# Kernel tuning notes

Hardware: AMD Instinct MI355X
Metric: run time of the kernel (lower is better)

## Reference

```python
import jax, jax.numpy as jnp
import numpy as np

NEG_SLOPE = 0.2  # PyG GATConv default


def gat_layer(x, W, att_src, att_dst, bias, src, dst, num_nodes, heads, out_ch):
    # x: [N, Fin]; W: [Fin, heads*out_ch]; att_*: [heads, out_ch]; bias: [heads*out_ch]
    xw = (x @ W).reshape(num_nodes, heads, out_ch)          # [N, H, C]
    a_src = jnp.sum(xw * att_src, axis=-1)                  # [N, H]
    a_dst = jnp.sum(xw * att_dst, axis=-1)                  # [N, H]
    e = jax.nn.leaky_relu(a_src[src] + a_dst[dst], NEG_SLOPE)  # [E, H]
    # segment softmax over incoming edges of each destination node
    e_max = jax.ops.segment_max(e, dst, num_segments=num_nodes)   # [N, H]
    e_exp = jnp.exp(e - e_max[dst])                                # [E, H]
    denom = jax.ops.segment_sum(e_exp, dst, num_segments=num_nodes)
    alpha = e_exp / denom[dst]                                     # [E, H]
    out = jax.ops.segment_sum(alpha[:, :, None] * xw[src], dst, num_segments=num_nodes)  # [N, H, C]
    return out.reshape(num_nodes, heads * out_ch) + bias


def setup_inputs() -> dict:
    key = jax.random.key(0)
    ks = jax.random.split(key, 12)
    N, E = 50000, 800000
    F_IN, HID, HEADS, NCLS = 128, 32, 4, 8
    x = jax.random.normal(ks[0], (N, F_IN), dtype=jnp.float32)
    src = jax.random.randint(ks[1], (E,), 0, N)
    dst = jax.random.randint(ks[2], (E,), 0, N)
    dst = jnp.where(dst == src, (dst + 1) % N, dst)  # no self loops; reference adds them
    edge_index = jnp.stack([src, dst]).astype(jnp.int64)
    s1 = 1.0 / np.sqrt(F_IN)
    s2 = 1.0 / np.sqrt(HEADS * HID)
    W1 = jax.random.normal(ks[3], (F_IN, HEADS * HID), dtype=jnp.float32) * s1
    att_src1 = jax.random.normal(ks[4], (HEADS, HID), dtype=jnp.float32) * s2
    att_dst1 = jax.random.normal(ks[5], (HEADS, HID), dtype=jnp.float32) * s2
    b1 = jnp.zeros((HEADS * HID,), dtype=jnp.float32)
    W2 = jax.random.normal(ks[6], (HEADS * HID, NCLS), dtype=jnp.float32) * s2
    att_src2 = jax.random.normal(ks[7], (1, NCLS), dtype=jnp.float32)
    att_dst2 = jax.random.normal(ks[8], (1, NCLS), dtype=jnp.float32)
    b2 = jnp.zeros((NCLS,), dtype=jnp.float32)
    return {"x": x, "edge_index": edge_index, "W1": W1, "att_src1": att_src1,
            "att_dst1": att_dst1, "b1": b1, "W2": W2, "att_src2": att_src2,
            "att_dst2": att_dst2, "b2": b2}


def reference(x, edge_index, W1, att_src1, att_dst1, b1, W2, att_src2, att_dst2, b2):
    N = x.shape[0]
    loops = jnp.arange(N, dtype=edge_index.dtype)
    src = jnp.concatenate([edge_index[0], loops])  # add self loops (PyG default)
    dst = jnp.concatenate([edge_index[1], loops])
    h = gat_layer(x, W1, att_src1, att_dst1, b1, src, dst, N, heads=4, out_ch=32)
    h = jax.nn.relu(h)
    out = gat_layer(h, W2, att_src2, att_dst2, b2, src, dst, N, heads=1, out_ch=8)
    return jax.nn.log_softmax(out, axis=1)
```

## Files before the change

kernel.cpp:

```cpp
#include <hip/hip_runtime.h>
#include <hip/hip_fp16.h>
#include <math.h>

#define F_IN   128
#define HEADS  4
#define HID    32
#define NCLS   8
#define SLOPE  0.2f
#define CAP    64
#define NBK    256
#define BSH    8
#define CHK    4096
#define BCAP   5120

typedef _Float16 half8 __attribute__((ext_vector_type(8)));
typedef float    floatx4 __attribute__((ext_vector_type(4)));
typedef float    floatv4 __attribute__((ext_vector_type(4)));

__global__ void k_prep(int* __restrict__ bcur,
                       const float* __restrict__ W1, _Float16* __restrict__ Wt) {
    if (blockIdx.x == 0) {
        bcur[threadIdx.x] = threadIdx.x * BCAP;
    } else {
        int idx = (blockIdx.x - 1) * 256 + threadIdx.x;
        int c = idx >> 7, k = idx & 127;
        Wt[c * 128 + k] = (_Float16)W1[k * 128 + c];
    }
}

__global__ void k_scatter(const int* __restrict__ ei, int* __restrict__ bcur,
                          unsigned* __restrict__ stage, int E) {
    __shared__ int hist[NBK];
    __shared__ int lcur[NBK];
    hist[threadIdx.x] = 0;
    int probe = ei[2 * (threadIdx.x & 63) + 1];
    bool is64 = (__ballot(probe != 0) == 0ULL);
    __syncthreads();
    int base = blockIdx.x * CHK;
    int dd[16], ss[16];
    #pragma unroll
    for (int k = 0; k < 16; k++) {
        int i = base + k * 256 + threadIdx.x;
        if (i < E) {
            dd[k] = is64 ? ei[2 * E + 2 * i] : ei[E + i];
            ss[k] = is64 ? ei[2 * i]         : ei[i];
            atomicAdd(&hist[dd[k] >> BSH], 1);
        } else dd[k] = -1;
    }
    __syncthreads();
    {
        int h = hist[threadIdx.x];
        lcur[threadIdx.x] = (h > 0) ? atomicAdd(&bcur[threadIdx.x], h) : 0;
    }
    __syncthreads();
    #pragma unroll
    for (int k = 0; k < 16; k++) {
        if (dd[k] >= 0) {
            int bkt = dd[k] >> BSH;
            int p = atomicAdd(&lcur[bkt], 1);
            if (p < (bkt + 1) * BCAP)
                stage[p] = ((unsigned)dd[k] << 16) | (unsigned)ss[k];
        }
    }
}

__global__ void k_bucket_gemm(const unsigned* __restrict__ stage,
                              const int* __restrict__ bcur,
                              unsigned short* __restrict__ csr16, int* __restrict__ cur,
                              int N,
                              const float* __restrict__ x, const _Float16* __restrict__ Wt,
                              const float* __restrict__ as1, const float* __restrict__ ad1,
                              _Float16* __restrict__ xwh, float* __restrict__ asrc,
                              float* __restrict__ adst) {
    if ((int)blockIdx.x < NBK) {
        int b  = blockIdx.x;
        int lo = b << BSH;
        if (lo >= N) return;
        int nn = N - lo; if (nn > 256) nn = 256;
        __shared__ int lc[256];
        lc[threadIdx.x] = (threadIdx.x < nn) ? 1 : 0;
        __syncthreads();
        if (threadIdx.x < nn)
            csr16[(size_t)(lo + threadIdx.x) * CAP] = (unsigned short)(lo + threadIdx.x);
        int base = b * BCAP;
        int cnt  = bcur[b] - base;
        if (cnt > BCAP) cnt = BCAP;
        if (cnt < 0) cnt = 0;
        for (int i = base + threadIdx.x; i < base + cnt; i += 256) {
            unsigned u = stage[i];
            int d = u >> 16, s = u & 0xFFFF;
            int p = atomicAdd(&lc[d - lo], 1);
            if (p < CAP) csr16[(size_t)d * CAP + p] = (unsigned short)s;
        }
        __syncthreads();
        if (threadIdx.x < nn) {
            int c = lc[threadIdx.x];
            cur[lo + threadIdx.x] = (c > CAP) ? CAP : c;
        }
        return;
    }
    int gb   = blockIdx.x - NBK;
    int wv   = threadIdx.x >> 6;
    int lane = threadIdx.x & 63;
    int r0   = gb * 64 + wv * 16;
    if (r0 >= N) return;
    int q = lane >> 4, t = lane & 15;
    int row = r0 + t;
    bool rok = row < N;

    half8 afr[4];
    #pragma unroll
    for (int kc = 0; kc < 4; kc++) {
        floatv4 u0 = {0.f, 0.f, 0.f, 0.f}, u1 = u0;
        if (rok) {
            const floatv4* xr = (const floatv4*)(x + (size_t)row * 128 + kc * 32 + q * 8);
            u0 = __builtin_nontemporal_load(xr);
            u1 = __builtin_nontemporal_load(xr + 1);
        }
        afr[kc][0] = (_Float16)u0[0]; afr[kc][1] = (_Float16)u0[1];
        afr[kc][2] = (_Float16)u0[2]; afr[kc][3] = (_Float16)u0[3];
        afr[kc][4] = (_Float16)u1[0]; afr[kc][5] = (_Float16)u1[1];
        afr[kc][6] = (_Float16)u1[2]; afr[kc][7] = (_Float16)u1[3];
    }

    float ps[4], pd[4];
    #pragma unroll
    for (int ct = 0; ct < 8; ct++) {
        floatx4 acc = {0.f, 0.f, 0.f, 0.f};
        #pragma unroll
        for (int kc = 0; kc < 4; kc++) {
            half8 bfr = *(const half8*)(Wt + (ct * 16 + t) * 128 + kc * 32 + q * 8);
            acc = __builtin_amdgcn_mfma_f32_16x16x32_f16(afr[kc], bfr, acc, 0, 0, 0);
        }
        int col = ct * 16 + t;
        float sa = as1[col], da = ad1[col];
        if ((ct & 1) == 0) {
            #pragma unroll
            for (int g = 0; g < 4; g++) { ps[g] = 0.f; pd[g] = 0.f; }
        }
        #pragma unroll
        for (int g = 0; g < 4; g++) {
            int r = r0 + q * 4 + g;
            if (r < N)
                __builtin_nontemporal_store((_Float16)acc[g], xwh + (size_t)r * 128 + col);
            ps[g] += acc[g] * sa;
            pd[g] += acc[g] * da;
        }
        if (ct & 1) {
            int h = ct >> 1;
            #pragma unroll
            for (int g = 0; g < 4; g++) {
                float a = ps[g], d = pd[g];
                a += __shfl_xor(a, 1); d += __shfl_xor(d, 1);
                a += __shfl_xor(a, 2); d += __shfl_xor(d, 2);
                a += __shfl_xor(a, 4); d += __shfl_xor(d, 4);
                a += __shfl_xor(a, 8); d += __shfl_xor(d, 8);
                int r = r0 + q * 4 + g;
                if (t == 0 && r < N) { asrc[r * 4 + h] = a; adst[r * 4 + h] = d; }
            }
        }
    }
}

__global__ void k_agg1(const _Float16* __restrict__ xwh, const float* __restrict__ asrc,
                       const float* __restrict__ adst, const int* __restrict__ cur,
                       const unsigned short* __restrict__ csr16, const float* __restrict__ b1,
                       const float* __restrict__ W2, const float* __restrict__ as2,
                       const float* __restrict__ ad2, float* __restrict__ xw2,
                       float* __restrict__ asrc2, float* __restrict__ adst2, int N) {
    int node = (blockIdx.x * blockDim.x + threadIdx.x) >> 6;
    int lane = threadIdx.x & 63;
    if (node >= N) return;
    int h = lane >> 4;
    int t = lane & 15;
    int ch = h * 32 + 2 * t;

    const float4* w2p = (const float4*)(W2 + ch * 8);
    float4 wa0 = w2p[0], wa1 = w2p[1];
    float4 wb0 = w2p[2], wb1 = w2p[3];
    float a_s = as2[lane & 7];
    float a_d = ad2[lane & 7];

    float adst_h = adst[node * 4 + h];
    int beg = node * CAP;
    int deg = cur[node];
    int end = beg + deg;

    float s = 0.f, a0 = 0.f, a1 = 0.f;
    int j = beg;
    for (; j + 8 <= end; j += 8) {
        ushort4 sA = *(const ushort4*)(csr16 + j);
        ushort4 sB = *(const ushort4*)(csr16 + j + 4);
        float e0 = asrc[sA.x * 4 + h] + adst_h;
        float e1 = asrc[sA.y * 4 + h] + adst_h;
        float e2 = asrc[sA.z * 4 + h] + adst_h;
        float e3 = asrc[sA.w * 4 + h] + adst_h;
        float e4 = asrc[sB.x * 4 + h] + adst_h;
        float e5 = asrc[sB.y * 4 + h] + adst_h;
        float e6 = asrc[sB.z * 4 + h] + adst_h;
        float e7 = asrc[sB.w * 4 + h] + adst_h;
        float2 f0 = __half22float2(*(const __half2*)(xwh + (size_t)sA.x * 128 + ch));
        float2 f1 = __half22float2(*(const __half2*)(xwh + (size_t)sA.y * 128 + ch));
        float2 f2 = __half22float2(*(const __half2*)(xwh + (size_t)sA.z * 128 + ch));
        float2 f3 = __half22float2(*(const __half2*)(xwh + (size_t)sA.w * 128 + ch));
        float2 f4 = __half22float2(*(const __half2*)(xwh + (size_t)sB.x * 128 + ch));
        float2 f5 = __half22float2(*(const __half2*)(xwh + (size_t)sB.y * 128 + ch));
        float2 f6 = __half22float2(*(const __half2*)(xwh + (size_t)sB.z * 128 + ch));
        float2 f7 = __half22float2(*(const __half2*)(xwh + (size_t)sB.w * 128 + ch));
        e0 = (e0 > 0.f) ? e0 : SLOPE * e0;   float p0 = __expf(e0);
        e1 = (e1 > 0.f) ? e1 : SLOPE * e1;   float p1 = __expf(e1);
        e2 = (e2 > 0.f) ? e2 : SLOPE * e2;   float p2 = __expf(e2);
        e3 = (e3 > 0.f) ? e3 : SLOPE * e3;   float p3 = __expf(e3);
        e4 = (e4 > 0.f) ? e4 : SLOPE * e4;   float p4 = __expf(e4);
        e5 = (e5 > 0.f) ? e5 : SLOPE * e5;   float p5 = __expf(e5);
        e6 = (e6 > 0.f) ? e6 : SLOPE * e6;   float p6 = __expf(e6);
        e7 = (e7 > 0.f) ? e7 : SLOPE * e7;   float p7 = __expf(e7);
        s  += (p0 + p1 + p2 + p3) + (p4 + p5 + p6 + p7);
        a0 += p0 * f0.x + p1 * f1.x + p2 * f2.x + p3 * f3.x
            + p4 * f4.x + p5 * f5.x + p6 * f6.x + p7 * f7.x;
        a1 += p0 * f0.y + p1 * f1.y + p2 * f2.y + p3 * f3.y
            + p4 * f4.y + p5 * f5.y + p6 * f6.y + p7 * f7.y;
    }
    for (; j < end; j++) {
        int s0 = csr16[j];
        float e0 = asrc[s0 * 4 + h] + adst_h;
        float2 f0 = __half22float2(*(const __half2*)(xwh + (size_t)s0 * 128 + ch));
        e0 = (e0 > 0.f) ? e0 : SLOPE * e0;
        float p0 = __expf(e0);
        s  += p0;
        a0 += p0 * f0.x;
        a1 += p0 * f0.y;
    }
    float inv = 1.f / s;
    float o0 = fmaxf(a0 * inv + b1[ch],     0.f);
    float o1 = fmaxf(a1 * inv + b1[ch + 1], 0.f);

    float p[8];
    p[0] = o0 * wa0.x + o1 * wb0.x;  p[1] = o0 * wa0.y + o1 * wb0.y;
    p[2] = o0 * wa0.z + o1 * wb0.z;  p[3] = o0 * wa0.w + o1 * wb0.w;
    p[4] = o0 * wa1.x + o1 * wb1.x;  p[5] = o0 * wa1.y + o1 * wb1.y;
    p[6] = o0 * wa1.z + o1 * wb1.z;  p[7] = o0 * wa1.w + o1 * wb1.w;
    float qq[4];
    #pragma unroll
    for (int b = 0; b < 4; b++) {
        float keepv = (lane & 1) ? p[2 * b + 1] : p[2 * b];
        float sendv = (lane & 1) ? p[2 * b]     : p[2 * b + 1];
        qq[b] = keepv + __shfl_xor(sendv, 1);
    }
    float r2[2];
    #pragma unroll
    for (int b = 0; b < 2; b++) {
        float keepv = (lane & 2) ? qq[2 * b + 1] : qq[2 * b];
        float sendv = (lane & 2) ? qq[2 * b]     : qq[2 * b + 1];
        r2[b] = keepv + __shfl_xor(sendv, 2);
    }
    {
        float keepv = (lane & 4) ? r2[1] : r2[0];
        float sendv = (lane & 4) ? r2[0] : r2[1];
        r2[0] = keepv + __shfl_xor(sendv, 4);
    }
    float f = r2[0];
    f += __shfl_xor(f, 8);
    f += __shfl_xor(f, 16);
    f += __shfl_xor(f, 32);
    if (lane < 8) xw2[node * 8 + lane] = f;
    float vs = f * a_s;
    float vd = f * a_d;
    vs += __shfl_xor(vs, 1); vs += __shfl_xor(vs, 2); vs += __shfl_xor(vs, 4);
    vd += __shfl_xor(vd, 1); vd += __shfl_xor(vd, 2); vd += __shfl_xor(vd, 4);
    if (lane == 0) { asrc2[node] = vs; adst2[node] = vd; }
}

__global__ void k_agg2(const float* __restrict__ xw2, const float* __restrict__ asrc2,
                       const float* __restrict__ adst2, const int* __restrict__ cur,
                       const unsigned short* __restrict__ csr16, const float* __restrict__ b2,
                       float* __restrict__ out, int N) {
    int node = (blockIdx.x * blockDim.x + threadIdx.x) >> 6;
    int lane = threadIdx.x & 63;
    if (node >= N) return;
    int slot = lane >> 3;
    int c    = lane & 7;
    float adst = adst2[node];
    int beg = node * CAP;
    int deg = cur[node];
    float s = 0.f, acc = 0.f;
    for (int j = slot; j < deg; j += 8) {
        int s0 = csr16[beg + j];
        float e0 = asrc2[s0] + adst;
        float v0 = xw2[s0 * 8 + c];
        e0 = (e0 > 0.f) ? e0 : SLOPE * e0;
        float p0 = __expf(e0);
        s   += p0;
        acc += p0 * v0;
    }
    #pragma unroll
    for (int mk = 8; mk < 64; mk <<= 1) {
        s   += __shfl_xor(s, mk);
        acc += __shfl_xor(acc, mk);
    }
    float o = acc / s + b2[c];
    float mxv = o;
    mxv = fmaxf(mxv, __shfl_xor(mxv, 1));
    mxv = fmaxf(mxv, __shfl_xor(mxv, 2));
    mxv = fmaxf(mxv, __shfl_xor(mxv, 4));
    float ex = __expf(o - mxv);
    float se = ex;
    se += __shfl_xor(se, 1); se += __shfl_xor(se, 2); se += __shfl_xor(se, 4);
    if (slot == 0) out[node * 8 + c] = o - mxv - __logf(se);
}

extern "C" void kernel_launch(void* const* d_in, const int* in_sizes, int n_in,
                              void* d_out, int out_size, void* d_ws, size_t ws_size,
                              hipStream_t stream) {
    const float* x   = (const float*)d_in[0];
    const int*   ei  = (const int*)d_in[1];
    const float* W1  = (const float*)d_in[2];
    const float* as1 = (const float*)d_in[3];
    const float* ad1 = (const float*)d_in[4];
    const float* b1  = (const float*)d_in[5];
    const float* W2  = (const float*)d_in[6];
    const float* as2 = (const float*)d_in[7];
    const float* ad2 = (const float*)d_in[8];
    const float* b2  = (const float*)d_in[9];
    float* out = (float*)d_out;

    int N = in_sizes[0] / F_IN;
    int E = in_sizes[1] / 2;
    int GB   = (N + 63) / 64;
    int NCHK = (E + CHK - 1) / CHK;

    char* p = (char*)d_ws;
    auto carve = [&](size_t bytes) { char* q = p; p += (bytes + 255) & ~(size_t)255; return (void*)q; };
    _Float16* xw1h = (_Float16*)carve((size_t)N * 128 * 2);
    _Float16* Wt   = (_Float16*)carve(128 * 128 * 2);
    float* asrc1 = (float*)carve((size_t)N * 4 * 4);
    float* adst1 = (float*)carve((size_t)N * 4 * 4);
    float* xw2   = (float*)carve((size_t)N * 8 * 4);
    float* asrc2 = (float*)carve((size_t)N * 4);
    float* adst2 = (float*)carve((size_t)N * 4);
    int*   cur   = (int*)carve((size_t)N * 4);
    int*   bcur  = (int*)carve(NBK * 4);
    unsigned* stage = (unsigned*)carve((size_t)NBK * BCAP * 4);
    unsigned short* csr16 = (unsigned short*)carve((size_t)N * CAP * 2);

    k_prep<<<65, 256, 0, stream>>>(bcur, W1, Wt);
    k_scatter<<<NCHK, 256, 0, stream>>>(ei, bcur, stage, E);
    k_bucket_gemm<<<NBK + GB, 256, 0, stream>>>(stage, bcur, csr16, cur, N,
                                                x, Wt, as1, ad1, xw1h, asrc1, adst1);
    k_agg1<<<(N + 3) / 4, 256, 0, stream>>>(xw1h, asrc1, adst1, cur, csr16, b1,
                                            W2, as2, ad2, xw2, asrc2, adst2, N);
    k_agg2<<<(N + 3) / 4, 256, 0, stream>>>(xw2, asrc2, adst2, cur, csr16, b2, out, N);
}
```

Measured before the change: 206.8 us.

## Co-schedule edge scatter with layer-1 GEMM and stage GEMM output via LDS

```diff
diff --git a/kernel.cpp b/kernel.cpp
--- a/kernel.cpp
+++ b/kernel.cpp
@@ -12,6 +12,7 @@
 #define BSH    8
 #define CHK    4096
 #define BCAP   5120
+#define SSTR   136
 
 typedef _Float16 half8 __attribute__((ext_vector_type(8)));
 typedef float    floatx4 __attribute__((ext_vector_type(4)));
@@ -28,78 +29,49 @@
     }
 }
 
-__global__ void k_scatter(const int* __restrict__ ei, int* __restrict__ bcur,
-                          unsigned* __restrict__ stage, int E) {
-    __shared__ int hist[NBK];
-    __shared__ int lcur[NBK];
-    hist[threadIdx.x] = 0;
-    int probe = ei[2 * (threadIdx.x & 63) + 1];
-    bool is64 = (__ballot(probe != 0) == 0ULL);
-    __syncthreads();
-    int base = blockIdx.x * CHK;
-    int dd[16], ss[16];
-    #pragma unroll
-    for (int k = 0; k < 16; k++) {
-        int i = base + k * 256 + threadIdx.x;
-        if (i < E) {
-            dd[k] = is64 ? ei[2 * E + 2 * i] : ei[E + i];
-            ss[k] = is64 ? ei[2 * i]         : ei[i];
-            atomicAdd(&hist[dd[k] >> BSH], 1);
-        } else dd[k] = -1;
-    }
-    __syncthreads();
-    {
-        int h = hist[threadIdx.x];
-        lcur[threadIdx.x] = (h > 0) ? atomicAdd(&bcur[threadIdx.x], h) : 0;
-    }
-    __syncthreads();
-    #pragma unroll
-    for (int k = 0; k < 16; k++) {
-        if (dd[k] >= 0) {
-            int bkt = dd[k] >> BSH;
-            int p = atomicAdd(&lcur[bkt], 1);
-            if (p < (bkt + 1) * BCAP)
-                stage[p] = ((unsigned)dd[k] << 16) | (unsigned)ss[k];
-        }
-    }
-}
-
-__global__ void k_bucket_gemm(const unsigned* __restrict__ stage,
-                              const int* __restrict__ bcur,
-                              unsigned short* __restrict__ csr16, int* __restrict__ cur,
-                              int N,
-                              const float* __restrict__ x, const _Float16* __restrict__ Wt,
-                              const float* __restrict__ as1, const float* __restrict__ ad1,
-                              _Float16* __restrict__ xwh, float* __restrict__ asrc,
-                              float* __restrict__ adst) {
-    if ((int)blockIdx.x < NBK) {
-        int b  = blockIdx.x;
-        int lo = b << BSH;
-        if (lo >= N) return;
-        int nn = N - lo; if (nn > 256) nn = 256;
-        __shared__ int lc[256];
-        lc[threadIdx.x] = (threadIdx.x < nn) ? 1 : 0;
+__global__ void k_scatter_gemm(const int* __restrict__ ei, int* __restrict__ bcur,
+                               unsigned* __restrict__ stage, int E, int N, int NCHK,
+                               const float* __restrict__ x, const _Float16* __restrict__ Wt,
+                               const float* __restrict__ as1, const float* __restrict__ ad1,
+                               _Float16* __restrict__ xwh, float* __restrict__ asrc,
+                               float* __restrict__ adst) {
+    __shared__ __align__(16) unsigned char smem[4 * 16 * SSTR * 2];
+    if ((int)blockIdx.x < NCHK) {
+        int* hist = (int*)smem;
+        int* lcur = hist + NBK;
+        hist[threadIdx.x] = 0;
+        int probe = ei[2 * (threadIdx.x & 63) + 1];
+        bool is64 = (__ballot(probe != 0) == 0ULL);
         __syncthreads();
-        if (threadIdx.x < nn)
-            csr16[(size_t)(lo + threadIdx.x) * CAP] = (unsigned short)(lo + threadIdx.x);
-        int base = b * BCAP;
-        int cnt  = bcur[b] - base;
-        if (cnt > BCAP) cnt = BCAP;
-        if (cnt < 0) cnt = 0;
-        for (int i = base + threadIdx.x; i < base + cnt; i += 256) {
-            unsigned u = stage[i];
-            int d = u >> 16, s = u & 0xFFFF;
-            int p = atomicAdd(&lc[d - lo], 1);
-            if (p < CAP) csr16[(size_t)d * CAP + p] = (unsigned short)s;
+        int base = blockIdx.x * CHK;
+        int dd[16], ss[16];
+        #pragma unroll
+        for (int k = 0; k < 16; k++) {
+            int i = base + k * 256 + threadIdx.x;
+            if (i < E) {
+                dd[k] = is64 ? ei[2 * E + 2 * i] : ei[E + i];
+                ss[k] = is64 ? ei[2 * i]         : ei[i];
+                atomicAdd(&hist[dd[k] >> BSH], 1);
+            } else dd[k] = -1;
         }
         __syncthreads();
-        if (threadIdx.x < nn) {
-            int c = lc[threadIdx.x];
-            cur[lo + threadIdx.x] = (c > CAP) ? CAP : c;
+        {
+            int h = hist[threadIdx.x];
+            lcur[threadIdx.x] = (h > 0) ? atomicAdd(&bcur[threadIdx.x], h) : 0;
+        }
+        __syncthreads();
+        #pragma unroll
+        for (int k = 0; k < 16; k++) {
+            if (dd[k] >= 0) {
+                int bkt = dd[k] >> BSH;
+                int p = atomicAdd(&lcur[bkt], 1);
+                if (p < (bkt + 1) * BCAP)
+                    stage[p] = ((unsigned)dd[k] << 16) | (unsigned)ss[k];
+            }
         }
         return;
     }
-    int gb   = blockIdx.x - NBK;
+    int gb   = blockIdx.x - NCHK;
     int wv   = threadIdx.x >> 6;
     int lane = threadIdx.x & 63;
     int r0   = gb * 64 + wv * 16;
@@ -107,6 +79,7 @@
     int q = lane >> 4, t = lane & 15;
     int row = r0 + t;
     bool rok = row < N;
+    _Float16* shw = (_Float16*)smem + wv * (16 * SSTR);
 
     half8 afr[4];
     #pragma unroll
@@ -140,9 +113,7 @@
         }
         #pragma unroll
         for (int g = 0; g < 4; g++) {
-            int r = r0 + q * 4 + g;
-            if (r < N)
-                __builtin_nontemporal_store((_Float16)acc[g], xwh + (size_t)r * 128 + col);
+            shw[(q * 4 + g) * SSTR + col] = (_Float16)acc[g];
             ps[g] += acc[g] * sa;
             pd[g] += acc[g] * da;
         }
@@ -159,6 +130,42 @@
                 if (t == 0 && r < N) { asrc[r * 4 + h] = a; adst[r * 4 + h] = d; }
             }
         }
+    }
+    #pragma unroll
+    for (int k = 0; k < 4; k++) {
+        int idx = k * 64 + lane;
+        int rr = idx >> 4, cc = idx & 15;
+        if (r0 + rr < N)
+            *(half8*)(xwh + (size_t)(r0 + rr) * 128 + cc * 8) =
+                *(const half8*)(shw + rr * SSTR + cc * 8);
+    }
+}
+
+__global__ void k_fill(const unsigned* __restrict__ stage, const int* __restrict__ bcur,
+                       unsigned short* __restrict__ csr16, int* __restrict__ cur, int N) {
+    int b  = blockIdx.x;
+    int lo = b << BSH;
+    if (lo >= N) return;
+    int nn = N - lo; if (nn > 256) nn = 256;
+    __shared__ int lc[256];
+    lc[threadIdx.x] = (threadIdx.x < nn) ? 1 : 0;
+    __syncthreads();
+    if (threadIdx.x < nn)
+        csr16[(size_t)(lo + threadIdx.x) * CAP] = (unsigned short)(lo + threadIdx.x);
+    int base = b * BCAP;
+    int cnt  = bcur[b] - base;
+    if (cnt > BCAP) cnt = BCAP;
+    if (cnt < 0) cnt = 0;
+    for (int i = base + threadIdx.x; i < base + cnt; i += 256) {
+        unsigned u = stage[i];
+        int d = u >> 16, s = u & 0xFFFF;
+        int p = atomicAdd(&lc[d - lo], 1);
+        if (p < CAP) csr16[(size_t)d * CAP + p] = (unsigned short)s;
+    }
+    __syncthreads();
+    if (threadIdx.x < nn) {
+        int c = lc[threadIdx.x];
+        cur[lo + threadIdx.x] = (c > CAP) ? CAP : c;
     }
 }
 
@@ -344,9 +351,9 @@
     unsigned short* csr16 = (unsigned short*)carve((size_t)N * CAP * 2);
 
     k_prep<<<65, 256, 0, stream>>>(bcur, W1, Wt);
-    k_scatter<<<NCHK, 256, 0, stream>>>(ei, bcur, stage, E);
-    k_bucket_gemm<<<NBK + GB, 256, 0, stream>>>(stage, bcur, csr16, cur, N,
-                                                x, Wt, as1, ad1, xw1h, asrc1, adst1);
+    k_scatter_gemm<<<NCHK + GB, 256, 0, stream>>>(ei, bcur, stage, E, N, NCHK,
+                                                  x, Wt, as1, ad1, xw1h, asrc1, adst1);
+    k_fill<<<NBK, 256, 0, stream>>>(stage, bcur, csr16, cur, N);
     k_agg1<<<(N + 3) / 4, 256, 0, stream>>>(xw1h, asrc1, adst1, cur, csr16, b1,
                                             W2, as2, ad2, xw2, asrc2, adst2, N);
     k_agg2<<<(N + 3) / 4, 256, 0, stream>>>(xw2, asrc2, adst2, cur, csr16, b2, out, N);
```

Result: faster. 197.1 us (-4.7%).
